# Optimization experiments

Hardware: AMD Instinct MI355X
Metric: run time of the kernel (lower is better)

## Reference

```python
import jax, jax.numpy as jnp
import numpy as np

B, H, W, C = 64, 14, 14, 768
HID = 4 * C            # ConvNeXt MLP hidden
E, K, R = 8, 2, 16     # num_experts, top_k, lora rank
SCALING = 16.0 / 16.0  # alpha / r


def setup_inputs() -> dict:
    key = jax.random.key(0)
    ks = jax.random.split(key, 9)
    N = B * H * W
    x = jax.random.normal(ks[0], (B, H, W, C), jnp.float32)
    p = jax.random.uniform(ks[1], (N, K), jnp.float32)
    topk_probs = p / (p.sum(-1, keepdims=True) + 1e-6)
    topk_idx = jax.random.randint(ks[2], (N, K), 0, E)
    w1 = jax.random.normal(ks[3], (C, HID), jnp.float32) * (C ** -0.5)
    b1 = jnp.zeros((HID,), jnp.float32)
    w2 = jax.random.normal(ks[4], (HID, C), jnp.float32) * (HID ** -0.5)
    b2 = jnp.zeros((C,), jnp.float32)
    w_down = jax.random.normal(ks[5], (E, C, R), jnp.float32) * (C ** -0.5)
    # torch init is zeros; use small randn so the op is numerically non-trivial
    w_up = jax.random.normal(ks[6], (E, R, C), jnp.float32) * 0.02
    return {"x": x, "topk_probs": topk_probs, "topk_idx": topk_idx,
            "w1": w1, "b1": b1, "w2": w2, "b2": b2,
            "w_down": w_down, "w_up": w_up}


def reference(x, topk_probs, topk_idx, w1, b1, w2, b2, w_down, w_up):
    # orig ConvNeXt MLP: Linear -> GELU(exact) -> Linear, pointwise over [B,H,W,C]
    h = jax.nn.gelu(jnp.einsum('bhwc,cf->bhwf', x, w1) + b1, approximate=False)
    orig = jnp.einsum('bhwf,fc->bhwc', h, w2) + b2

    N = x.shape[0] * x.shape[1] * x.shape[2]
    xf = x.reshape(N, C)  # [N, C] tokens
    # per-token combine weight for each expert: sum_k p[n,k] * 1[idx[n,k]==e]
    wt = (jax.nn.one_hot(topk_idx, E, dtype=xf.dtype) * topk_probs[..., None]).sum(1)  # [N, E]
    # dense-over-experts LoRA (vectorized form of the per-expert gather/scatter loop)
    down = jax.nn.gelu(jnp.einsum('nc,ecr->ner', xf, w_down), approximate=False)  # [N, E, R]
    up = jnp.einsum('ner,erc->nec', down, w_up) * SCALING                          # [N, E, C]
    moe = jnp.einsum('nec,ne->nc', up, wt)                                         # [N, C]
    return orig + moe.reshape(x.shape)
```

## Files before the change

### kernel.cpp

```cpp
#include <hip/hip_runtime.h>
#include <hip/hip_bf16.h>
#include <math.h>


#define NTOK   12544
#define CDIM   768
#define HIDDIM 3072
#define KBIG   3200

typedef __attribute__((ext_vector_type(8))) short bf16x8;
typedef __attribute__((ext_vector_type(4))) float f32x4;

#define GLOBAL_AS(p) ((const __attribute__((address_space(1))) void*)(p))
#define LDS_AS(p)    ((__attribute__((address_space(3))) void*)(p))
#define GLD(src, dst) __builtin_amdgcn_global_load_lds(GLOBAL_AS(src), LDS_AS(dst), 16, 0, 0)

__device__ inline unsigned short f2bf(float f) {
    unsigned int x = __float_as_uint(f);
    x += 0x7fffu + ((x >> 16) & 1u);
    return (unsigned short)(x >> 16);
}

__device__ inline float gelu_fast(float x) {
    float x3 = x * x * x;
    float u2 = 1.5957691216057308f * x + 0.07135481627260025f * x3;
    float e = __expf(-u2);
    return x * __builtin_amdgcn_rcpf(1.0f + e);
}

__global__ void __launch_bounds__(256) prep_kernel(
        const float* __restrict__ x, const float* __restrict__ w1,
        const float* __restrict__ w2, const float* __restrict__ wup,
        const float* __restrict__ wdn,
        unsigned short* __restrict__ xb, unsigned short* __restrict__ w1t,
        unsigned short* __restrict__ B2t, unsigned short* __restrict__ wdt) {
    __shared__ float tile[64][65];
    const int b = blockIdx.x, tid = threadIdx.x;
    if (b < 9408) {
        int i = b * 256 + tid;
        float4 v = ((const float4*)x)[i];
        ushort4 o;
        o.x = f2bf(v.x); o.y = f2bf(v.y); o.z = f2bf(v.z); o.w = f2bf(v.w);
        ((ushort4*)xb)[i] = o;
        return;
    }
    if (b < 10584) {
        const float* in; unsigned short* outp; int Ccols, out_ld, out_off, bx, by;
        if (b < 9984)       { int t = b - 9408;  in = w1;  outp = w1t; Ccols = 3072; out_ld = 768;  out_off = 0;    bx = t % 48; by = t / 48; }
        else if (b < 10560) { int t = b - 9984;  in = w2;  outp = B2t; Ccols = 768;  out_ld = 3200; out_off = 0;    bx = t % 12; by = t / 12; }
        else                { int t = b - 10560; in = wup; outp = B2t; Ccols = 768;  out_ld = 3200; out_off = 3072; bx = t % 12; by = t / 12; }
        const int c0 = bx * 64, r0 = by * 64;
        #pragma unroll
        for (int p = 0; p < 4; ++p) {
            int idx = p * 256 + tid;
            int r = idx >> 4, c4 = (idx & 15) * 4;
            float4 v = *(const float4*)&in[(size_t)(r0 + r) * Ccols + c0 + c4];
            tile[r][c4 + 0] = v.x; tile[r][c4 + 1] = v.y;
            tile[r][c4 + 2] = v.z; tile[r][c4 + 3] = v.w;
        }
        __syncthreads();
        #pragma unroll
        for (int p = 0; p < 2; ++p) {
            int u = p * 256 + tid;
            int cc = u >> 3, r8 = (u & 7) * 8;
            uint4 pk;
            pk.x = (unsigned)f2bf(tile[r8 + 0][cc]) | ((unsigned)f2bf(tile[r8 + 1][cc]) << 16);
            pk.y = (unsigned)f2bf(tile[r8 + 2][cc]) | ((unsigned)f2bf(tile[r8 + 3][cc]) << 16);
            pk.z = (unsigned)f2bf(tile[r8 + 4][cc]) | ((unsigned)f2bf(tile[r8 + 5][cc]) << 16);
            pk.w = (unsigned)f2bf(tile[r8 + 6][cc]) | ((unsigned)f2bf(tile[r8 + 7][cc]) << 16);
            *(uint4*)&outp[(size_t)(c0 + cc) * out_ld + out_off + r0 + r8] = pk;
        }
        return;
    }
    {
        int idx = (b - 10584) * 256 + tid;
        int j = idx / 768, c = idx - j * 768;
        int e = j >> 4, r = j & 15;
        wdt[idx] = f2bf(wdn[((size_t)e * 768 + c) * 16 + r]);
    }
}

template <int EPI, int TM>
__global__ void __launch_bounds__(TM * 2)
gemm_bt_kernel(const unsigned short* __restrict__ A, int lda,
               const unsigned short* __restrict__ Bt, int ldb,
               int kIters,
               const float* __restrict__ bias,
               unsigned short* __restrict__ apOut,
               float* __restrict__ fOut,
               const int* __restrict__ tki,
               const float* __restrict__ tkp) {
    constexpr int NT    = TM * 2;
    constexpr int ABUF  = TM * 32;
    constexpr int BBUF  = 128 * 32;
    __shared__ __align__(16) unsigned short As[2 * ABUF];
    __shared__ __align__(16) unsigned short Bs[2 * BBUF];

    const int bx = blockIdx.x, by = blockIdx.y;
    const int tid  = threadIdx.x;
    const int wave = tid >> 6;
    const int lane = tid & 63;
    const int m0 = by * TM;
    const int n0 = bx * 128;
    const int wm = (wave >> 1) * 64;
    const int wn = (wave & 1) * 64;
    const int row16 = lane & 15;
    const int quad  = lane >> 4;
    const int kch   = quad * 8;

    f32x4 acc[4][4] = {};

    const int r_s = tid >> 2;
    const int c_s = (tid & 3) * 8;
    const size_t aRow0 = (size_t)(m0 + r_s) * lda + c_s;
    const size_t aRow1 = aRow0 + (size_t)(NT / 4) * lda;
    const size_t bRow0 = (size_t)(n0 + r_s) * ldb + c_s;
    const size_t bRow1 = bRow0 + (size_t)64 * ldb;
    unsigned short* asB0 = &As[(wave * 64) * 8];
    unsigned short* asB1 = &As[(NT + wave * 64) * 8];
    unsigned short* bsB0 = &Bs[(wave * 64) * 8];
    unsigned short* bsB1 = &Bs[(256 + wave * 64) * 8];

    {
        GLD(A + aRow0, asB0);
        GLD(A + aRow1, asB1);
        GLD(Bt + bRow0, bsB0);
        if (TM == 128) GLD(Bt + bRow1, bsB1);
    }

    for (int kt = 0; kt < kIters; ++kt) {
        __syncthreads();

        if (kt + 1 < kIters) {
            const int k1 = (kt + 1) * 32;
            const int pa = ((kt + 1) & 1) * ABUF;
            const int pb = ((kt + 1) & 1) * BBUF;
            GLD(A + aRow0 + k1, asB0 + pa);
            GLD(A + aRow1 + k1, asB1 + pa);
            GLD(Bt + bRow0 + k1, bsB0 + pb);
            if (TM == 128) GLD(Bt + bRow1 + k1, bsB1 + pb);
        }

        const int ca = (kt & 1) * ABUF;
        const int cb = (kt & 1) * BBUF;
        bf16x8 af[4], bfr[4];
        #pragma unroll
        for (int mi = 0; mi < 4; ++mi)
            af[mi] = *(const bf16x8*)&As[ca + (wm + mi * 16 + row16) * 32 + kch];
        #pragma unroll
        for (int ni = 0; ni < 4; ++ni)
            bfr[ni] = *(const bf16x8*)&Bs[cb + (wn + ni * 16 + row16) * 32 + kch];

        #pragma unroll
        for (int mi = 0; mi < 4; ++mi)
            #pragma unroll
            for (int ni = 0; ni < 4; ++ni)
                acc[mi][ni] = __builtin_amdgcn_mfma_f32_16x16x32_bf16(
                    af[mi], bfr[ni], acc[mi][ni], 0, 0, 0);
    }

    #pragma unroll
    for (int mi = 0; mi < 4; ++mi) {
        #pragma unroll
        for (int i = 0; i < 4; ++i) {
            const int m = m0 + wm + mi * 16 + quad * 4 + i;
            int i0 = 0, i1 = 0; float p0 = 0.f, p1 = 0.f;
            if (EPI == 1) {
                i0 = tki[m * 2]; i1 = tki[m * 2 + 1];
                p0 = tkp[m * 2]; p1 = tkp[m * 2 + 1];
            }
            #pragma unroll
            for (int ni = 0; ni < 4; ++ni) {
                const int ncol = n0 + wn + ni * 16 + row16;
                float v = acc[mi][ni][i];
                if (EPI == 0) {
                    v = gelu_fast(v + bias[ncol]);
                    apOut[(size_t)m * KBIG + ncol] = f2bf(v);
                } else if (EPI == 1) {
                    const int e = ncol >> 4;
                    float wt = (i0 == e ? p0 : 0.f) + (i1 == e ? p1 : 0.f);
                    v = gelu_fast(v) * wt;
                    apOut[(size_t)m * KBIG + 3072 + ncol] = f2bf(v);
                } else {
                    fOut[(size_t)m * CDIM + ncol] = v + bias[ncol];
                }
            }
        }
    }
}


template <int Q, bool TAILV, class Issue>
__device__ __forceinline__ void phase8(
        const char* ldsAbuf, const char* ldsBbuf, int aFB, int bFB, int swz,
        f32x4 (&acc)[8][4], bf16x8 (&bfr)[4][2], Issue issue) {
    bf16x8 af[2][2];
    #pragma unroll
    for (int f = 0; f < 2; ++f)
        #pragma unroll
        for (int k = 0; k < 2; ++k)
            af[f][k] = *(const bf16x8*)(ldsAbuf + ((aFB + Q * 4096 + f * 2048 + k * 64) ^ swz));
    if (Q == 0) {
        #pragma unroll
        for (int nf = 0; nf < 4; ++nf)
            #pragma unroll
            for (int k = 0; k < 2; ++k)
                bfr[nf][k] = *(const bf16x8*)(ldsBbuf + ((bFB + nf * 2048 + k * 64) ^ swz));
    }
    issue();
    __builtin_amdgcn_s_barrier();
    asm volatile("s_waitcnt lgkmcnt(0)" ::: "memory");
    __builtin_amdgcn_sched_barrier(0);
    __builtin_amdgcn_s_setprio(1);
    #pragma unroll
    for (int f = 0; f < 2; ++f)
        #pragma unroll
        for (int nf = 0; nf < 4; ++nf)
            #pragma unroll
            for (int k = 0; k < 2; ++k)
                acc[2 * Q + f][nf] = __builtin_amdgcn_mfma_f32_16x16x32_bf16(
                    af[f][k], bfr[nf][k], acc[2 * Q + f][nf], 0, 0, 0);
    __builtin_amdgcn_s_setprio(0);
    if (TAILV) asm volatile("s_waitcnt vmcnt(4)" ::: "memory");
    __builtin_amdgcn_s_barrier();
    __builtin_amdgcn_sched_barrier(0);
}

template <int EPI>
__global__ void __launch_bounds__(512, 2)
gemm8_kernel(const unsigned short* __restrict__ A, int lda,
             const unsigned short* __restrict__ Bt, int ldb,
             int kTiles, const float* __restrict__ bias,
             unsigned short* __restrict__ apOut, float* __restrict__ fOut) {
    __shared__ __align__(1024) unsigned short ldsbuf[65536];
    char* ldsA = (char*)ldsbuf;
    char* ldsB = (char*)ldsbuf + 65536;

    const int tid  = threadIdx.x;
    const int wave = tid >> 6;
    const int lane = tid & 63;
    const int m0 = blockIdx.y * 256;
    const int n0 = blockIdx.x * 256;
    const int row16 = lane & 15;
    const int quad  = lane >> 4;
    const int wm = (wave >> 2) << 7;
    const int wn = (wave & 3) << 6;
    const int swz = (row16 & 7) << 4;
    const int aFB = ((wm + row16) << 7) + (quad << 4);
    const int bFB = ((wn + row16) << 7) + (quad << 4);

    const int d  = tid << 4;
    const int s  = d ^ (((d >> 7) & 7) << 4);
    const int sr = s >> 7;
    const int sc = (s & 127) >> 1;
    const char* aSrc = (const char*)(A + (size_t)(m0 + sr) * lda + sc);
    const char* bSrc = (const char*)(Bt + (size_t)(n0 + sr) * ldb + sc);
    const size_t aPass = (size_t)64 * lda * 2, aHalf = aPass * 2;
    const size_t bPass = (size_t)64 * ldb * 2, bHalf = bPass * 2;
    const int ldsW = wave << 10;

    auto issueA = [&](int b, int h, int tk) {
        const char* sp = aSrc + (size_t)h * aHalf + (size_t)tk * 128;
        char* dp = ldsA + b * 32768 + h * 16384 + ldsW;
        GLD(sp, dp);
        GLD(sp + aPass, dp + 8192);
    };
    auto issueB = [&](int b, int h, int tk) {
        const char* sp = bSrc + (size_t)h * bHalf + (size_t)tk * 128;
        char* dp = ldsB + b * 32768 + h * 16384 + ldsW;
        GLD(sp, dp);
        GLD(sp + bPass, dp + 8192);
    };

    f32x4 acc[8][4] = {};

    issueB(0, 0, 0); issueB(0, 1, 0);
    issueA(0, 0, 0); issueA(0, 1, 0);
    issueB(1, 0, 1); issueB(1, 1, 1);
    asm volatile("s_waitcnt vmcnt(4)" ::: "memory");
    __builtin_amdgcn_s_barrier();
    __builtin_amdgcn_sched_barrier(0);

    const char* A0 = ldsA;         const char* B0 = ldsB;
    const char* A1 = ldsA + 32768; const char* B1 = ldsB + 32768;
    const int nIter = kTiles >> 1;
    for (int it = 0; it < nIter; ++it) {
        const int t  = it * 2;
        const int t2 = (t + 2 < kTiles) ? t + 2 : 0;
        const int t3 = (t + 3 < kTiles) ? t + 3 : 0;
        bf16x8 bfr[4][2];
        phase8<0, false>(A0, B0, aFB, bFB, swz, acc, bfr, [&]{ issueA(1, 0, t + 1); });
        phase8<1, false>(A0, B0, aFB, bFB, swz, acc, bfr, [&]{ issueA(1, 1, t + 1); });
        phase8<2, false>(A0, B0, aFB, bFB, swz, acc, bfr, [&]{ issueB(0, 0, t2); });
        phase8<3, true >(A0, B0, aFB, bFB, swz, acc, bfr, [&]{ issueB(0, 1, t2); });
        phase8<0, false>(A1, B1, aFB, bFB, swz, acc, bfr, [&]{ issueA(0, 0, t2); });
        phase8<1, false>(A1, B1, aFB, bFB, swz, acc, bfr, [&]{ issueA(0, 1, t2); });
        phase8<2, false>(A1, B1, aFB, bFB, swz, acc, bfr, [&]{ issueB(1, 0, t3); });
        phase8<3, true >(A1, B1, aFB, bFB, swz, acc, bfr, [&]{ issueB(1, 1, t3); });
    }
    asm volatile("s_waitcnt vmcnt(0)" ::: "memory");

    float bv[4];
    #pragma unroll
    for (int nf = 0; nf < 4; ++nf) bv[nf] = bias[n0 + wn + nf * 16 + row16];
    #pragma unroll
    for (int mi = 0; mi < 8; ++mi) {
        #pragma unroll
        for (int i = 0; i < 4; ++i) {
            const int m = m0 + wm + mi * 16 + quad * 4 + i;
            #pragma unroll
            for (int nf = 0; nf < 4; ++nf) {
                const int col = n0 + wn + nf * 16 + row16;
                float v = acc[mi][nf][i] + bv[nf];
                if (EPI == 0) apOut[(size_t)m * KBIG + col] = f2bf(gelu_fast(v));
                else          fOut[(size_t)m * CDIM + col] = v;
            }
        }
    }
}


extern "C" void kernel_launch(void* const* d_in, const int* in_sizes, int n_in,
                              void* d_out, int out_size, void* d_ws, size_t ws_size,
                              hipStream_t stream) {
    const float* x   = (const float*)d_in[0];
    const float* tkp = (const float*)d_in[1];
    const int*   tki = (const int*)d_in[2];
    const float* w1  = (const float*)d_in[3];
    const float* b1  = (const float*)d_in[4];
    const float* w2  = (const float*)d_in[5];
    const float* b2  = (const float*)d_in[6];
    const float* wdn = (const float*)d_in[7];
    const float* wup = (const float*)d_in[8];
    float* out = (float*)d_out;

    unsigned short* xb  = (unsigned short*)d_ws;
    unsigned short* w1t = xb  + (size_t)NTOK * CDIM;
    unsigned short* B2t = w1t + (size_t)HIDDIM * CDIM;
    unsigned short* wdt = B2t + (size_t)CDIM * KBIG;
    unsigned short* Ap  = wdt + (size_t)128 * CDIM;

    prep_kernel<<<dim3(10968), 256, 0, stream>>>(x, w1, w2, wup, wdn,
                                                 xb, w1t, B2t, wdt);

    gemm_bt_kernel<1, 128><<<dim3(1, NTOK / 128), 256, 0, stream>>>(
        xb, CDIM, wdt, CDIM, CDIM / 32, nullptr, Ap, nullptr, tki, tkp);
    gemm8_kernel<0><<<dim3(HIDDIM / 256, NTOK / 256), 512, 0, stream>>>(
        xb, CDIM, w1t, CDIM, CDIM / 64, b1, Ap, nullptr);
    gemm8_kernel<2><<<dim3(CDIM / 256, NTOK / 256), 512, 0, stream>>>(
        Ap, KBIG, B2t, KBIG, KBIG / 64, b2, nullptr, out);
}
```

Before: 286.3 us.

## Use 256x192 tiles for second GEMM and XCD-aware block remapping

The 8-wave GEMM kernel is templated on the number of N fragments so the second GEMM (N=768) can use 256x192 tiles. That gives 4 column tiles times 49 row tiles, 196 blocks instead of 147, to fill more of the CUs. The grid is flattened to 1D and block IDs are remapped so consecutive logical tiles land on the same XCD, improving L2 reuse. The B load schedule and vmcnt waits are adjusted for the 3-fragment case. This risks lower MFMA density per wave and mismatched wait counts.

```diff
diff --git a/kernel.cpp b/kernel.cpp
--- a/kernel.cpp
+++ b/kernel.cpp
@@ -190,10 +190,10 @@
 }
 
 
-template <int Q, bool TAILV, class Issue>
+template <int NFRAG, int Q, bool TAILV, class Issue>
 __device__ __forceinline__ void phase8(
         const char* ldsAbuf, const char* ldsBbuf, int aFB, int bFB, int swz,
-        f32x4 (&acc)[8][4], bf16x8 (&bfr)[4][2], Issue issue) {
+        f32x4 (&acc)[8][NFRAG], bf16x8 (&bfr)[NFRAG][2], Issue issue) {
     bf16x8 af[2][2];
     #pragma unroll
     for (int f = 0; f < 2; ++f)
@@ -202,7 +202,7 @@
             af[f][k] = *(const bf16x8*)(ldsAbuf + ((aFB + Q * 4096 + f * 2048 + k * 64) ^ swz));
     if (Q == 0) {
         #pragma unroll
-        for (int nf = 0; nf < 4; ++nf)
+        for (int nf = 0; nf < NFRAG; ++nf)
             #pragma unroll
             for (int k = 0; k < 2; ++k)
                 bfr[nf][k] = *(const bf16x8*)(ldsBbuf + ((bFB + nf * 2048 + k * 64) ^ swz));
@@ -215,36 +215,47 @@
     #pragma unroll
     for (int f = 0; f < 2; ++f)
         #pragma unroll
-        for (int nf = 0; nf < 4; ++nf)
+        for (int nf = 0; nf < NFRAG; ++nf)
             #pragma unroll
             for (int k = 0; k < 2; ++k)
                 acc[2 * Q + f][nf] = __builtin_amdgcn_mfma_f32_16x16x32_bf16(
                     af[f][k], bfr[nf][k], acc[2 * Q + f][nf], 0, 0, 0);
     __builtin_amdgcn_s_setprio(0);
-    if (TAILV) asm volatile("s_waitcnt vmcnt(4)" ::: "memory");
+    if (TAILV) {
+        if constexpr (NFRAG == 4) asm volatile("s_waitcnt vmcnt(4)" ::: "memory");
+        else                      asm volatile("s_waitcnt vmcnt(3)" ::: "memory");
+    }
     __builtin_amdgcn_s_barrier();
     __builtin_amdgcn_sched_barrier(0);
 }
 
-template <int EPI>
+template <int EPI, int NFRAG, int NBX>
 __global__ void __launch_bounds__(512, 2)
 gemm8_kernel(const unsigned short* __restrict__ A, int lda,
              const unsigned short* __restrict__ Bt, int ldb,
              int kTiles, const float* __restrict__ bias,
              unsigned short* __restrict__ apOut, float* __restrict__ fOut) {
-    __shared__ __align__(1024) unsigned short ldsbuf[65536];
-    char* ldsA = (char*)ldsbuf;
-    char* ldsB = (char*)ldsbuf + 65536;
+    constexpr int BBYTES = NFRAG * 8192;
+    __shared__ __align__(1024) char ldsraw[65536 + 2 * BBYTES];
+    char* ldsA = ldsraw;
+    char* ldsB = ldsraw + 65536;
+
+    const int nwg  = gridDim.x;
+    const int q    = nwg >> 3, r = nwg & 7;
+    const int orig = blockIdx.x;
+    const int xcd  = orig & 7, within = orig >> 3;
+    const int wgid = (xcd < r ? xcd * (q + 1) : r * (q + 1) + (xcd - r) * q) + within;
+    const int bx = wgid % NBX, by = wgid / NBX;
 
     const int tid  = threadIdx.x;
     const int wave = tid >> 6;
     const int lane = tid & 63;
-    const int m0 = blockIdx.y * 256;
-    const int n0 = blockIdx.x * 256;
+    const int m0 = by * 256;
+    const int n0 = bx * (NFRAG * 64);
     const int row16 = lane & 15;
     const int quad  = lane >> 4;
     const int wm = (wave >> 2) << 7;
-    const int wn = (wave & 3) << 6;
+    const int wn = (wave & 3) * (NFRAG * 16);
     const int swz = (row16 & 7) << 4;
     const int aFB = ((wm + row16) << 7) + (quad << 4);
     const int bFB = ((wn + row16) << 7) + (quad << 4);
@@ -255,61 +266,67 @@
     const int sc = (s & 127) >> 1;
     const char* aSrc = (const char*)(A + (size_t)(m0 + sr) * lda + sc);
     const char* bSrc = (const char*)(Bt + (size_t)(n0 + sr) * ldb + sc);
-    const size_t aPass = (size_t)64 * lda * 2, aHalf = aPass * 2;
-    const size_t bPass = (size_t)64 * ldb * 2, bHalf = bPass * 2;
+    const size_t aStep = (size_t)64 * lda * 2;
+    const size_t bStep = (size_t)64 * ldb * 2;
     const int ldsW = wave << 10;
 
     auto issueA = [&](int b, int h, int tk) {
-        const char* sp = aSrc + (size_t)h * aHalf + (size_t)tk * 128;
+        const char* sp = aSrc + (size_t)(2 * h) * aStep + (size_t)tk * 128;
         char* dp = ldsA + b * 32768 + h * 16384 + ldsW;
         GLD(sp, dp);
-        GLD(sp + aPass, dp + 8192);
+        GLD(sp + aStep, dp + 8192);
     };
-    auto issueB = [&](int b, int h, int tk) {
-        const char* sp = bSrc + (size_t)h * bHalf + (size_t)tk * 128;
-        char* dp = ldsB + b * 32768 + h * 16384 + ldsW;
+    auto issueB = [&](int b, int c, int tk) {
+        const char* sp = bSrc + (size_t)c * bStep + (size_t)tk * 128;
+        char* dp = ldsB + b * BBYTES + c * 8192 + ldsW;
         GLD(sp, dp);
-        GLD(sp + bPass, dp + 8192);
     };
 
-    f32x4 acc[8][4] = {};
-
-    issueB(0, 0, 0); issueB(0, 1, 0);
+    f32x4 acc[8][NFRAG] = {};
+
+    #pragma unroll
+    for (int c = 0; c < NFRAG; ++c) issueB(0, c, 0);
     issueA(0, 0, 0); issueA(0, 1, 0);
-    issueB(1, 0, 1); issueB(1, 1, 1);
-    asm volatile("s_waitcnt vmcnt(4)" ::: "memory");
+    #pragma unroll
+    for (int c = 0; c < NFRAG; ++c) issueB(1, c, 1);
+    if constexpr (NFRAG == 4) asm volatile("s_waitcnt vmcnt(4)" ::: "memory");
+    else                      asm volatile("s_waitcnt vmcnt(3)" ::: "memory");
     __builtin_amdgcn_s_barrier();
     __builtin_amdgcn_sched_barrier(0);
 
     const char* A0 = ldsA;         const char* B0 = ldsB;
-    const char* A1 = ldsA + 32768; const char* B1 = ldsB + 32768;
+    const char* A1 = ldsA + 32768; const char* B1 = ldsB + BBYTES;
     const int nIter = kTiles >> 1;
     for (int it = 0; it < nIter; ++it) {
         const int t  = it * 2;
         const int t2 = (t + 2 < kTiles) ? t + 2 : 0;
         const int t3 = (t + 3 < kTiles) ? t + 3 : 0;
-        bf16x8 bfr[4][2];
-        phase8<0, false>(A0, B0, aFB, bFB, swz, acc, bfr, [&]{ issueA(1, 0, t + 1); });
-        phase8<1, false>(A0, B0, aFB, bFB, swz, acc, bfr, [&]{ issueA(1, 1, t + 1); });
-        phase8<2, false>(A0, B0, aFB, bFB, swz, acc, bfr, [&]{ issueB(0, 0, t2); });
-        phase8<3, true >(A0, B0, aFB, bFB, swz, acc, bfr, [&]{ issueB(0, 1, t2); });
-        phase8<0, false>(A1, B1, aFB, bFB, swz, acc, bfr, [&]{ issueA(0, 0, t2); });
-        phase8<1, false>(A1, B1, aFB, bFB, swz, acc, bfr, [&]{ issueA(0, 1, t2); });
-        phase8<2, false>(A1, B1, aFB, bFB, swz, acc, bfr, [&]{ issueB(1, 0, t3); });
-        phase8<3, true >(A1, B1, aFB, bFB, swz, acc, bfr, [&]{ issueB(1, 1, t3); });
+        bf16x8 bfr[NFRAG][2];
+        phase8<NFRAG, 0, false>(A0, B0, aFB, bFB, swz, acc, bfr, [&]{ issueA(1, 0, t + 1); });
+        phase8<NFRAG, 1, false>(A0, B0, aFB, bFB, swz, acc, bfr, [&]{ issueA(1, 1, t + 1); });
+        phase8<NFRAG, 2, false>(A0, B0, aFB, bFB, swz, acc, bfr, [&]{ issueB(0, 0, t2); issueB(0, 1, t2); });
+        phase8<NFRAG, 3, true >(A0, B0, aFB, bFB, swz, acc, bfr, [&]{
+            #pragma unroll
+            for (int c = 2; c < NFRAG; ++c) issueB(0, c, t2); });
+        phase8<NFRAG, 0, false>(A1, B1, aFB, bFB, swz, acc, bfr, [&]{ issueA(0, 0, t2); });
+        phase8<NFRAG, 1, false>(A1, B1, aFB, bFB, swz, acc, bfr, [&]{ issueA(0, 1, t2); });
+        phase8<NFRAG, 2, false>(A1, B1, aFB, bFB, swz, acc, bfr, [&]{ issueB(1, 0, t3); issueB(1, 1, t3); });
+        phase8<NFRAG, 3, true >(A1, B1, aFB, bFB, swz, acc, bfr, [&]{
+            #pragma unroll
+            for (int c = 2; c < NFRAG; ++c) issueB(1, c, t3); });
     }
     asm volatile("s_waitcnt vmcnt(0)" ::: "memory");
 
-    float bv[4];
-    #pragma unroll
-    for (int nf = 0; nf < 4; ++nf) bv[nf] = bias[n0 + wn + nf * 16 + row16];
+    float bv[NFRAG];
+    #pragma unroll
+    for (int nf = 0; nf < NFRAG; ++nf) bv[nf] = bias[n0 + wn + nf * 16 + row16];
     #pragma unroll
     for (int mi = 0; mi < 8; ++mi) {
         #pragma unroll
         for (int i = 0; i < 4; ++i) {
             const int m = m0 + wm + mi * 16 + quad * 4 + i;
             #pragma unroll
-            for (int nf = 0; nf < 4; ++nf) {
+            for (int nf = 0; nf < NFRAG; ++nf) {
                 const int col = n0 + wn + nf * 16 + row16;
                 float v = acc[mi][nf][i] + bv[nf];
                 if (EPI == 0) apOut[(size_t)m * KBIG + col] = f2bf(gelu_fast(v));
@@ -345,8 +362,8 @@
 
     gemm_bt_kernel<1, 128><<<dim3(1, NTOK / 128), 256, 0, stream>>>(
         xb, CDIM, wdt, CDIM, CDIM / 32, nullptr, Ap, nullptr, tki, tkp);
-    gemm8_kernel<0><<<dim3(HIDDIM / 256, NTOK / 256), 512, 0, stream>>>(
+    gemm8_kernel<0, 4, HIDDIM / 256><<<dim3((HIDDIM / 256) * (NTOK / 256)), 512, 0, stream>>>(
         xb, CDIM, w1t, CDIM, CDIM / 64, b1, Ap, nullptr);
-    gemm8_kernel<2><<<dim3(CDIM / 256, NTOK / 256), 512, 0, stream>>>(
+    gemm8_kernel<2, 3, CDIM / 192><<<dim3((CDIM / 192) * (NTOK / 256)), 512, 0, stream>>>(
         Ap, KBIG, B2t, KBIG, KBIG / 64, b2, nullptr, out);
 }
```

Measured after the change: 271.7 us. 1.05x faster.
